# Kernel tuning notes

Hardware: AMD Instinct MI355X
Metric: run time of the kernel (lower is better)

Reference implementation:

```python
import jax, jax.numpy as jnp
import numpy as np

N, D, B = 500000, 128, 2048

def setup_inputs() -> dict:
    key = jax.random.key(0)
    ks = jax.random.split(key, 7)
    x = jax.random.normal(ks[0], (N, D), dtype=jnp.float32)
    batch = jnp.sort(jax.random.randint(ks[1], (N,), 0, B)).astype(jnp.int64)
    s = 1.0 / np.sqrt(D)
    Wm = jax.random.uniform(ks[2], (D, D), jnp.float32, -s, s)  # xavier-ish
    fc1_w = jax.random.uniform(ks[3], (D // 4, D), jnp.float32, -s, s)
    fc1_b = jnp.zeros((D // 4,), jnp.float32)
    fc2_w = jax.random.uniform(ks[4], (D, D // 4), jnp.float32, -1/np.sqrt(D//4), 1/np.sqrt(D//4))
    fc2_b = jnp.zeros((D,), jnp.float32)
    return {"x": x, "batch": batch, "size": B, "Wm": Wm,
            "fc1_w": fc1_w, "fc1_b": fc1_b, "fc2_w": fc2_w, "fc2_b": fc2_b}

def reference(x, batch, size, Wm, fc1_w, fc1_b, fc2_w, fc2_b):
    batch = batch.astype(jnp.int32)
    # fc: Linear -> ReLU -> Linear -> Tanh
    attention = jnp.tanh(jax.nn.relu(x @ fc1_w.T + fc1_b) @ fc2_w.T + fc2_b)
    x2 = attention * x + x  # [N, D]
    # scatter_mean over graphs
    sums = jax.ops.segment_sum(x2, batch, num_segments=size)  # [B, D]
    cnt = jax.ops.segment_sum(jnp.ones((x2.shape[0],), x2.dtype), batch, num_segments=size)
    mean = sums / jnp.maximum(cnt, 1.0)[:, None]
    transformed_global = jnp.tanh(mean @ Wm)  # [B, D]
    coefs = jax.nn.sigmoid(jnp.sum(x2 * transformed_global[batch], axis=1))  # [N]
    weighted = coefs[:, None] * x2
    return jax.ops.segment_sum(weighted, batch, num_segments=size)  # [B, D]
```

## Files before the change

kernel.cpp:

```cpp
#include <hip/hip_runtime.h>
#include <math.h>

#define D 128
#define BLOCKS_AC 768
#define THREADS_AC 256

typedef short s8v __attribute__((ext_vector_type(8)));
typedef float f4v __attribute__((ext_vector_type(4)));

__device__ __forceinline__ float fast_tanh(float z) {
    float e = __expf(2.f * z);
    return 1.f - 2.f / (e + 1.f);
}
__device__ __forceinline__ unsigned short f2bf(float f) {
    union { float f; unsigned u; } v; v.f = f;
    unsigned r = v.u + 0x7FFFu + ((v.u >> 16) & 1u);
    return (unsigned short)(r >> 16);
}
__device__ __forceinline__ float bf2f(unsigned short h) {
    union { unsigned u; float f; } v; v.u = ((unsigned)h) << 16;
    return v.f;
}

#define EPI(RG_)                                                              \
    {                                                                         \
        int r = R + quad * 4 + RG_;                                           \
        int seg = batch[r];                                                   \
        float yv[8];                                                          \
        _Pragma("unroll")                                                     \
        for (int t = 0; t < 8; ++t) {                                         \
            float xf = bf2f(xw[(quad * 4 + RG_) * 136 + m15 + 16 * t]);       \
            float z = af[t][RG_] + b2l[t];                                    \
            yv[t] = xf * (1.f + fast_tanh(z));                                \
        }                                                                     \
        if (PHASE == 1) {                                                     \
            float dot = 0.f;                                                  \
            _Pragma("unroll")                                                 \
            for (int t = 0; t < 8; ++t)                                       \
                dot = fmaf(yv[t], tg[seg * 128 + m15 + 16 * t], dot);         \
            dot += __shfl_xor(dot, 1);                                        \
            dot += __shfl_xor(dot, 2);                                        \
            dot += __shfl_xor(dot, 4);                                        \
            dot += __shfl_xor(dot, 8);                                        \
            float coef = 1.f / (1.f + __expf(-dot));                          \
            _Pragma("unroll")                                                 \
            for (int t = 0; t < 8; ++t) yv[t] *= coef;                        \
        }                                                                     \
        if (seg != cur) {                                                     \
            if (cur >= 0) {                                                   \
                _Pragma("unroll")                                             \
                for (int t = 0; t < 8; ++t)                                   \
                    atomicAdd(&dst[cur * 128 + m15 + 16 * t], acc[t]);        \
                if (PHASE == 0 && m15 == 0) atomicAdd(&cnt[cur], acnt);       \
            }                                                                 \
            cur = seg;                                                        \
            _Pragma("unroll")                                                 \
            for (int t = 0; t < 8; ++t) acc[t] = yv[t];                       \
            acnt = 1.f;                                                       \
        } else {                                                              \
            _Pragma("unroll")                                                 \
            for (int t = 0; t < 8; ++t) acc[t] += yv[t];                      \
            acnt += 1.f;                                                      \
        }                                                                     \
    }

template <int PHASE>
__global__ __launch_bounds__(THREADS_AC, 2) void phaseAC(
    const float* __restrict__ x, const int* __restrict__ batch,
    const float* __restrict__ fc1_w, const float* __restrict__ fc1_b,
    const float* __restrict__ fc2_w, const float* __restrict__ fc2_b,
    const float* __restrict__ tg, float* __restrict__ dst,
    float* __restrict__ cnt, int N)
{
    __shared__ unsigned short xbf[4][16 * 136];
    __shared__ float hbuf[4][16 * 36];

    const int lane = threadIdx.x & 63;
    const int wv = threadIdx.x >> 6;
    const int m15 = lane & 15;
    const int quad = lane >> 4;

    s8v B1[2][4];
    #pragma unroll
    for (int t = 0; t < 2; ++t)
        #pragma unroll
        for (int kc = 0; kc < 4; ++kc) {
            const float* p = fc1_w + (16 * t + m15) * 128 + kc * 32 + quad * 8;
            float4 w0 = *(const float4*)p;
            float4 w1 = *(const float4*)(p + 4);
            s8v f;
            f[0] = (short)f2bf(w0.x); f[1] = (short)f2bf(w0.y);
            f[2] = (short)f2bf(w0.z); f[3] = (short)f2bf(w0.w);
            f[4] = (short)f2bf(w1.x); f[5] = (short)f2bf(w1.y);
            f[6] = (short)f2bf(w1.z); f[7] = (short)f2bf(w1.w);
            B1[t][kc] = f;
        }
    s8v B2[8];
    #pragma unroll
    for (int t = 0; t < 8; ++t) {
        const float* p = fc2_w + (16 * t + m15) * 32 + quad * 8;
        float4 w0 = *(const float4*)p;
        float4 w1 = *(const float4*)(p + 4);
        s8v f;
        f[0] = (short)f2bf(w0.x); f[1] = (short)f2bf(w0.y);
        f[2] = (short)f2bf(w0.z); f[3] = (short)f2bf(w0.w);
        f[4] = (short)f2bf(w1.x); f[5] = (short)f2bf(w1.y);
        f[6] = (short)f2bf(w1.z); f[7] = (short)f2bf(w1.w);
        B2[t] = f;
    }
    float b1l[2], b2l[8];
    #pragma unroll
    for (int t = 0; t < 2; ++t) b1l[t] = fc1_b[m15 + 16 * t];
    #pragma unroll
    for (int t = 0; t < 8; ++t) b2l[t] = fc2_b[m15 + 16 * t];

    const int total16 = N >> 4;
    const int nw = BLOCKS_AC * 4;
    const int gw = blockIdx.x * 4 + wv;
    const int wpb = (total16 + nw - 1) / nw;
    const int b0 = gw * wpb;
    const int b1e = min(total16, b0 + wpb);

    unsigned short* xw = xbf[wv];
    float* hw = hbuf[wv];

    float acc[8];
    #pragma unroll
    for (int t = 0; t < 8; ++t) acc[t] = 0.f;
    int cur = -1;
    float acnt = 0.f;
    const f4v z4 = {0.f, 0.f, 0.f, 0.f};

    for (int b = b0; b < b1e; ++b) {
        const int R = b << 4;
        const float* xp = x + R * 128;
        #pragma unroll
        for (int u = 0; u < 8; ++u) {
            float4 v = *(const float4*)(xp + u * 256 + lane * 4);
            unsigned lo = (unsigned)f2bf(v.x) | ((unsigned)f2bf(v.y) << 16);
            unsigned hi = (unsigned)f2bf(v.z) | ((unsigned)f2bf(v.w) << 16);
            int row = 2 * u + (lane >> 5);
            int col = (lane & 31) * 4;
            uint2 pk; pk.x = lo; pk.y = hi;
            *(uint2*)&xw[row * 136 + col] = pk;
        }
        s8v ax[4];
        #pragma unroll
        for (int kc = 0; kc < 4; ++kc)
            ax[kc] = *(const s8v*)&xw[m15 * 136 + kc * 32 + quad * 8];
        f4v accH[2];
        accH[0] = z4; accH[1] = z4;
        #pragma unroll
        for (int kc = 0; kc < 4; ++kc) {
            accH[0] = __builtin_amdgcn_mfma_f32_16x16x32_bf16(ax[kc], B1[0][kc], accH[0], 0, 0, 0);
            accH[1] = __builtin_amdgcn_mfma_f32_16x16x32_bf16(ax[kc], B1[1][kc], accH[1], 0, 0, 0);
        }
        #pragma unroll
        for (int t = 0; t < 2; ++t)
            #pragma unroll
            for (int rg = 0; rg < 4; ++rg) {
                float hv = fmaxf(accH[t][rg] + b1l[t], 0.f);
                hw[(quad * 4 + rg) * 36 + m15 + 16 * t] = hv;
            }
        const f4v h0 = *(const f4v*)&hw[m15 * 36 + quad * 8];
        const f4v h1 = *(const f4v*)&hw[m15 * 36 + quad * 8 + 4];
        s8v ah;
        ah[0] = (short)f2bf(h0[0]); ah[1] = (short)f2bf(h0[1]);
        ah[2] = (short)f2bf(h0[2]); ah[3] = (short)f2bf(h0[3]);
        ah[4] = (short)f2bf(h1[0]); ah[5] = (short)f2bf(h1[1]);
        ah[6] = (short)f2bf(h1[2]); ah[7] = (short)f2bf(h1[3]);
        f4v af[8];
        #pragma unroll
        for (int t = 0; t < 8; ++t)
            af[t] = __builtin_amdgcn_mfma_f32_16x16x32_bf16(ah, B2[t], z4, 0, 0, 0);

        EPI(0) EPI(1) EPI(2) EPI(3)
    }
    if (cur >= 0) {
        #pragma unroll
        for (int t = 0; t < 8; ++t)
            atomicAdd(&dst[cur * 128 + m15 + 16 * t], acc[t]);
        if (PHASE == 0 && m15 == 0) atomicAdd(&cnt[cur], acnt);
    }
}

__global__ __launch_bounds__(D, 8) void phaseB(
    const float* __restrict__ sums, const float* __restrict__ cnt,
    const float* __restrict__ Wm, float* __restrict__ tg)
{
    int b = blockIdx.x;
    int d = threadIdx.x;
    __shared__ float m[D];
    float inv = 1.f / fmaxf(cnt[b], 1.f);
    m[d] = sums[(b << 7) + d] * inv;
    __syncthreads();
    float acc = 0.f;
    #pragma unroll 8
    for (int k = 0; k < D; ++k)
        acc = fmaf(m[k], Wm[(k << 7) + d], acc);
    tg[(b << 7) + d] = fast_tanh(acc);
}

extern "C" void kernel_launch(void* const* d_in, const int* in_sizes, int n_in,
                              void* d_out, int out_size, void* d_ws, size_t ws_size,
                              hipStream_t stream) {
    const float* x     = (const float*)d_in[0];
    const int*   batch = (const int*)d_in[1];
    const float* Wm    = (const float*)d_in[3];
    const float* fc1_w = (const float*)d_in[4];
    const float* fc1_b = (const float*)d_in[5];
    const float* fc2_w = (const float*)d_in[6];
    const float* fc2_b = (const float*)d_in[7];
    float* out = (float*)d_out;

    int N = in_sizes[0] / D;
    int B = out_size / D;

    float* sums = (float*)d_ws;
    float* cnt  = sums + (size_t)B * D;
    float* tg   = cnt + B;

    hipMemsetAsync(d_ws, 0, ((size_t)B * D + B) * sizeof(float), stream);
    hipMemsetAsync(d_out, 0, (size_t)out_size * sizeof(float), stream);

    phaseAC<0><<<BLOCKS_AC, THREADS_AC, 0, stream>>>(
        x, batch, fc1_w, fc1_b, fc2_w, fc2_b, nullptr, sums, cnt, N);
    phaseB<<<B, D, 0, stream>>>(sums, cnt, Wm, tg);
    phaseAC<1><<<BLOCKS_AC, THREADS_AC, 0, stream>>>(
        x, batch, fc1_w, fc1_b, fc2_w, fc2_b, tg, out, nullptr, N);
}
```

Before: 480.5 us.

## Materialize x2 in bf16 so the second pass skips recomputing the MLP

Phase A now writes the attention-scaled x2 to workspace as packed bf16. A new lightweight phase C reads that instead of re-reading fp32 x and rerunning both MFMA layers, so the second pass moves roughly half the bytes and drops its matrix work. The change also adds hardware packed bf16 conversion, register prefetch of the next tile, and a balanced work split across waves. In exchange it adds a write of about 128 MB, relies on workspace being large enough, and rounds x2 to bf16 before the dot product and the final sum.

```diff
diff --git a/kernel.cpp b/kernel.cpp
--- a/kernel.cpp
+++ b/kernel.cpp
@@ -2,8 +2,9 @@
 #include <math.h>
 
 #define D 128
-#define BLOCKS_AC 768
-#define THREADS_AC 256
+#define BLOCKS_A 768
+#define BLOCKS_C 1024
+#define THREADS 256
 
 typedef short s8v __attribute__((ext_vector_type(8)));
 typedef float f4v __attribute__((ext_vector_type(4)));
@@ -12,17 +13,25 @@
     float e = __expf(2.f * z);
     return 1.f - 2.f / (e + 1.f);
 }
-__device__ __forceinline__ unsigned short f2bf(float f) {
-    union { float f; unsigned u; } v; v.f = f;
-    unsigned r = v.u + 0x7FFFu + ((v.u >> 16) & 1u);
-    return (unsigned short)(r >> 16);
+__device__ __forceinline__ unsigned cvt_pk_bf16(float lo, float hi) {
+    unsigned r;
+    asm("v_cvt_pk_bf16_f32 %0, %1, %2" : "=v"(r) : "v"(lo), "v"(hi));
+    return r;
 }
 __device__ __forceinline__ float bf2f(unsigned short h) {
     union { unsigned u; float f; } v; v.u = ((unsigned)h) << 16;
     return v.f;
 }
-
-#define EPI(RG_)                                                              \
+__device__ __forceinline__ s8v pack8(float4 w0, float4 w1) {
+    union { unsigned u[4]; s8v v; } r;
+    r.u[0] = cvt_pk_bf16(w0.x, w0.y);
+    r.u[1] = cvt_pk_bf16(w0.z, w0.w);
+    r.u[2] = cvt_pk_bf16(w1.x, w1.y);
+    r.u[3] = cvt_pk_bf16(w1.z, w1.w);
+    return r.v;
+}
+
+#define EPI0(RG_)                                                             \
     {                                                                         \
         int r = R + quad * 4 + RG_;                                           \
         int seg = batch[r];                                                   \
@@ -33,25 +42,18 @@
             float z = af[t][RG_] + b2l[t];                                    \
             yv[t] = xf * (1.f + fast_tanh(z));                                \
         }                                                                     \
-        if (PHASE == 1) {                                                     \
-            float dot = 0.f;                                                  \
-            _Pragma("unroll")                                                 \
-            for (int t = 0; t < 8; ++t)                                       \
-                dot = fmaf(yv[t], tg[seg * 128 + m15 + 16 * t], dot);         \
-            dot += __shfl_xor(dot, 1);                                        \
-            dot += __shfl_xor(dot, 2);                                        \
-            dot += __shfl_xor(dot, 4);                                        \
-            dot += __shfl_xor(dot, 8);                                        \
-            float coef = 1.f / (1.f + __expf(-dot));                          \
-            _Pragma("unroll")                                                 \
-            for (int t = 0; t < 8; ++t) yv[t] *= coef;                        \
-        }                                                                     \
+        union { unsigned u[4]; uint4 q; } pk;                                 \
+        pk.u[0] = cvt_pk_bf16(yv[0], yv[1]);                                  \
+        pk.u[1] = cvt_pk_bf16(yv[2], yv[3]);                                  \
+        pk.u[2] = cvt_pk_bf16(yv[4], yv[5]);                                  \
+        pk.u[3] = cvt_pk_bf16(yv[6], yv[7]);                                  \
+        ((uint4*)x2s)[(size_t)b * 256 + RG_ * 64 + lane] = pk.q;              \
         if (seg != cur) {                                                     \
             if (cur >= 0) {                                                   \
                 _Pragma("unroll")                                             \
                 for (int t = 0; t < 8; ++t)                                   \
-                    atomicAdd(&dst[cur * 128 + m15 + 16 * t], acc[t]);        \
-                if (PHASE == 0 && m15 == 0) atomicAdd(&cnt[cur], acnt);       \
+                    atomicAdd(&sums[cur * 128 + m15 + 16 * t], acc[t]);       \
+                if (m15 == 0) atomicAdd(&cnt[cur], acnt);                     \
             }                                                                 \
             cur = seg;                                                        \
             _Pragma("unroll")                                                 \
@@ -64,13 +66,12 @@
         }                                                                     \
     }
 
-template <int PHASE>
-__global__ __launch_bounds__(THREADS_AC, 2) void phaseAC(
+__global__ __launch_bounds__(THREADS, 2) void phaseA(
     const float* __restrict__ x, const int* __restrict__ batch,
     const float* __restrict__ fc1_w, const float* __restrict__ fc1_b,
     const float* __restrict__ fc2_w, const float* __restrict__ fc2_b,
-    const float* __restrict__ tg, float* __restrict__ dst,
-    float* __restrict__ cnt, int N)
+    float* __restrict__ sums, float* __restrict__ cnt,
+    unsigned short* __restrict__ x2s, int N)
 {
     __shared__ unsigned short xbf[4][16 * 136];
     __shared__ float hbuf[4][16 * 36];
@@ -86,27 +87,13 @@
         #pragma unroll
         for (int kc = 0; kc < 4; ++kc) {
             const float* p = fc1_w + (16 * t + m15) * 128 + kc * 32 + quad * 8;
-            float4 w0 = *(const float4*)p;
-            float4 w1 = *(const float4*)(p + 4);
-            s8v f;
-            f[0] = (short)f2bf(w0.x); f[1] = (short)f2bf(w0.y);
-            f[2] = (short)f2bf(w0.z); f[3] = (short)f2bf(w0.w);
-            f[4] = (short)f2bf(w1.x); f[5] = (short)f2bf(w1.y);
-            f[6] = (short)f2bf(w1.z); f[7] = (short)f2bf(w1.w);
-            B1[t][kc] = f;
+            B1[t][kc] = pack8(*(const float4*)p, *(const float4*)(p + 4));
         }
     s8v B2[8];
     #pragma unroll
     for (int t = 0; t < 8; ++t) {
         const float* p = fc2_w + (16 * t + m15) * 32 + quad * 8;
-        float4 w0 = *(const float4*)p;
-        float4 w1 = *(const float4*)(p + 4);
-        s8v f;
-        f[0] = (short)f2bf(w0.x); f[1] = (short)f2bf(w0.y);
-        f[2] = (short)f2bf(w0.z); f[3] = (short)f2bf(w0.w);
-        f[4] = (short)f2bf(w1.x); f[5] = (short)f2bf(w1.y);
-        f[6] = (short)f2bf(w1.z); f[7] = (short)f2bf(w1.w);
-        B2[t] = f;
+        B2[t] = pack8(*(const float4*)p, *(const float4*)(p + 4));
     }
     float b1l[2], b2l[8];
     #pragma unroll
@@ -115,11 +102,11 @@
     for (int t = 0; t < 8; ++t) b2l[t] = fc2_b[m15 + 16 * t];
 
     const int total16 = N >> 4;
-    const int nw = BLOCKS_AC * 4;
+    const int nw = BLOCKS_A * 4;
     const int gw = blockIdx.x * 4 + wv;
-    const int wpb = (total16 + nw - 1) / nw;
-    const int b0 = gw * wpb;
-    const int b1e = min(total16, b0 + wpb);
+    const int base = total16 / nw, rem = total16 % nw;
+    const int b0 = gw * base + (gw < rem ? gw : rem);
+    const int b1e = b0 + base + (gw < rem ? 1 : 0);
 
     unsigned short* xw = xbf[wv];
     float* hw = hbuf[wv];
@@ -131,18 +118,33 @@
     float acnt = 0.f;
     const f4v z4 = {0.f, 0.f, 0.f, 0.f};
 
+    float4 L[8];
+    if (b0 < b1e) {
+        const float* xp = x + (size_t)(b0 << 4) * D;
+        #pragma unroll
+        for (int u = 0; u < 8; ++u)
+            L[u] = *(const float4*)(xp + u * 256 + lane * 4);
+    }
+
     for (int b = b0; b < b1e; ++b) {
         const int R = b << 4;
-        const float* xp = x + R * 128;
+        uint2 P[8];
         #pragma unroll
         for (int u = 0; u < 8; ++u) {
-            float4 v = *(const float4*)(xp + u * 256 + lane * 4);
-            unsigned lo = (unsigned)f2bf(v.x) | ((unsigned)f2bf(v.y) << 16);
-            unsigned hi = (unsigned)f2bf(v.z) | ((unsigned)f2bf(v.w) << 16);
+            P[u].x = cvt_pk_bf16(L[u].x, L[u].y);
+            P[u].y = cvt_pk_bf16(L[u].z, L[u].w);
+        }
+        if (b + 1 < b1e) {
+            const float* xp = x + (size_t)((b + 1) << 4) * D;
+            #pragma unroll
+            for (int u = 0; u < 8; ++u)
+                L[u] = *(const float4*)(xp + u * 256 + lane * 4);
+        }
+        #pragma unroll
+        for (int u = 0; u < 8; ++u) {
             int row = 2 * u + (lane >> 5);
             int col = (lane & 31) * 4;
-            uint2 pk; pk.x = lo; pk.y = hi;
-            *(uint2*)&xw[row * 136 + col] = pk;
+            *(uint2*)&xw[row * 136 + col] = P[u];
         }
         s8v ax[4];
         #pragma unroll
@@ -164,23 +166,24 @@
             }
         const f4v h0 = *(const f4v*)&hw[m15 * 36 + quad * 8];
         const f4v h1 = *(const f4v*)&hw[m15 * 36 + quad * 8 + 4];
-        s8v ah;
-        ah[0] = (short)f2bf(h0[0]); ah[1] = (short)f2bf(h0[1]);
-        ah[2] = (short)f2bf(h0[2]); ah[3] = (short)f2bf(h0[3]);
-        ah[4] = (short)f2bf(h1[0]); ah[5] = (short)f2bf(h1[1]);
-        ah[6] = (short)f2bf(h1[2]); ah[7] = (short)f2bf(h1[3]);
+        union { unsigned u[4]; s8v v; } ahu;
+        ahu.u[0] = cvt_pk_bf16(h0[0], h0[1]);
+        ahu.u[1] = cvt_pk_bf16(h0[2], h0[3]);
+        ahu.u[2] = cvt_pk_bf16(h1[0], h1[1]);
+        ahu.u[3] = cvt_pk_bf16(h1[2], h1[3]);
+        s8v ah = ahu.v;
         f4v af[8];
         #pragma unroll
         for (int t = 0; t < 8; ++t)
             af[t] = __builtin_amdgcn_mfma_f32_16x16x32_bf16(ah, B2[t], z4, 0, 0, 0);
 
-        EPI(0) EPI(1) EPI(2) EPI(3)
+        EPI0(0) EPI0(1) EPI0(2) EPI0(3)
     }
     if (cur >= 0) {
         #pragma unroll
         for (int t = 0; t < 8; ++t)
-            atomicAdd(&dst[cur * 128 + m15 + 16 * t], acc[t]);
-        if (PHASE == 0 && m15 == 0) atomicAdd(&cnt[cur], acnt);
+            atomicAdd(&sums[cur * 128 + m15 + 16 * t], acc[t]);
+        if (m15 == 0) atomicAdd(&cnt[cur], acnt);
     }
 }
 
@@ -201,6 +204,86 @@
     tg[(b << 7) + d] = fast_tanh(acc);
 }
 
+__global__ __launch_bounds__(THREADS, 4) void phaseC(
+    const unsigned short* __restrict__ x2s, const int* __restrict__ batch,
+    const float* __restrict__ tg, float* __restrict__ out, int N)
+{
+    const int lane = threadIdx.x & 63;
+    const int wv = threadIdx.x >> 6;
+    const int m15 = lane & 15;
+    const int quad = lane >> 4;
+
+    const int total16 = N >> 4;
+    const int nw = BLOCKS_C * 4;
+    const int gw = blockIdx.x * 4 + wv;
+    const int base = total16 / nw, rem = total16 % nw;
+    const int b0 = gw * base + (gw < rem ? gw : rem);
+    const int b1e = b0 + base + (gw < rem ? 1 : 0);
+
+    float acc[8], tgv[8];
+    #pragma unroll
+    for (int t = 0; t < 8; ++t) { acc[t] = 0.f; tgv[t] = 0.f; }
+    int cur = -1;
+
+    uint4 PK[4];
+    if (b0 < b1e) {
+        const uint4* p = (const uint4*)x2s + (size_t)b0 * 256 + lane;
+        #pragma unroll
+        for (int rg = 0; rg < 4; ++rg) PK[rg] = p[rg * 64];
+    }
+
+    for (int b = b0; b < b1e; ++b) {
+        uint4 C[4];
+        #pragma unroll
+        for (int rg = 0; rg < 4; ++rg) C[rg] = PK[rg];
+        if (b + 1 < b1e) {
+            const uint4* p = (const uint4*)x2s + (size_t)(b + 1) * 256 + lane;
+            #pragma unroll
+            for (int rg = 0; rg < 4; ++rg) PK[rg] = p[rg * 64];
+        }
+        const int R = b << 4;
+        #pragma unroll
+        for (int rg = 0; rg < 4; ++rg) {
+            int seg = batch[R + quad * 4 + rg];
+            if (seg != cur) {
+                if (cur >= 0) {
+                    #pragma unroll
+                    for (int t = 0; t < 8; ++t)
+                        atomicAdd(&out[cur * 128 + m15 + 16 * t], acc[t]);
+                }
+                cur = seg;
+                #pragma unroll
+                for (int t = 0; t < 8; ++t) {
+                    tgv[t] = tg[seg * 128 + m15 + 16 * t];
+                    acc[t] = 0.f;
+                }
+            }
+            float xv[8];
+            unsigned w;
+            union { unsigned u; float f; } cv;
+            w = C[rg].x; cv.u = w << 16; xv[0] = cv.f; cv.u = w & 0xffff0000u; xv[1] = cv.f;
+            w = C[rg].y; cv.u = w << 16; xv[2] = cv.f; cv.u = w & 0xffff0000u; xv[3] = cv.f;
+            w = C[rg].z; cv.u = w << 16; xv[4] = cv.f; cv.u = w & 0xffff0000u; xv[5] = cv.f;
+            w = C[rg].w; cv.u = w << 16; xv[6] = cv.f; cv.u = w & 0xffff0000u; xv[7] = cv.f;
+            float dot = 0.f;
+            #pragma unroll
+            for (int t = 0; t < 8; ++t) dot = fmaf(xv[t], tgv[t], dot);
+            dot += __shfl_xor(dot, 1);
+            dot += __shfl_xor(dot, 2);
+            dot += __shfl_xor(dot, 4);
+            dot += __shfl_xor(dot, 8);
+            float coef = 1.f / (1.f + __expf(-dot));
+            #pragma unroll
+            for (int t = 0; t < 8; ++t) acc[t] = fmaf(coef, xv[t], acc[t]);
+        }
+    }
+    if (cur >= 0) {
+        #pragma unroll
+        for (int t = 0; t < 8; ++t)
+            atomicAdd(&out[cur * 128 + m15 + 16 * t], acc[t]);
+    }
+}
+
 extern "C" void kernel_launch(void* const* d_in, const int* in_sizes, int n_in,
                               void* d_out, int out_size, void* d_ws, size_t ws_size,
                               hipStream_t stream) {
@@ -219,13 +302,13 @@
     float* sums = (float*)d_ws;
     float* cnt  = sums + (size_t)B * D;
     float* tg   = cnt + B;
+    unsigned short* x2s = (unsigned short*)(tg + (size_t)B * D);
 
     hipMemsetAsync(d_ws, 0, ((size_t)B * D + B) * sizeof(float), stream);
     hipMemsetAsync(d_out, 0, (size_t)out_size * sizeof(float), stream);
 
-    phaseAC<0><<<BLOCKS_AC, THREADS_AC, 0, stream>>>(
-        x, batch, fc1_w, fc1_b, fc2_w, fc2_b, nullptr, sums, cnt, N);
+    phaseA<<<BLOCKS_A, THREADS, 0, stream>>>(
+        x, batch, fc1_w, fc1_b, fc2_w, fc2_b, sums, cnt, x2s, N);
     phaseB<<<B, D, 0, stream>>>(sums, cnt, Wm, tg);
-    phaseAC<1><<<BLOCKS_AC, THREADS_AC, 0, stream>>>(
-        x, batch, fc1_w, fc1_b, fc2_w, fc2_b, tg, out, nullptr, N);
-}
+    phaseC<<<BLOCKS_C, THREADS, 0, stream>>>(x2s, batch, tg, out, N);
+}
```

Result: faster. 465.5 us (-3.1%).
